# Performance work log

Hardware: AMD Instinct MI355X
Metric: run time of the kernel (lower is better)

Reference implementation:

```python
import jax, jax.numpy as jnp
import numpy as np

N_NODES = 50000
N_EDGES = 800000
N_GRAPHS = 64


def graph_conv(x, edge_index, w_rel, b_rel, w_root):
    # PyG GraphConv with aggr='add':
    #   out = lin_rel(sum_{j in N(i)} x_j) + lin_root(x_i)
    src, dst = edge_index[0], edge_index[1]
    agg = jax.ops.segment_sum(x[src], dst, num_segments=x.shape[0])  # [N, d_in]
    return agg @ w_rel + b_rel + x @ w_root  # [N, d_out]


def scatter_mean(x, batch, num_segments):
    s = jax.ops.segment_sum(x, batch, num_segments=num_segments)
    cnt = jax.ops.segment_sum(jnp.ones((x.shape[0],), x.dtype), batch,
                              num_segments=num_segments)
    return s / jnp.maximum(cnt, 1.0)[:, None]


def setup_inputs() -> dict:
    key = jax.random.key(0)
    ks = jax.random.split(key, 8)
    d_feat, d_hid, d_out = 128, 128, 128
    x = jax.random.normal(ks[0], (N_NODES, d_feat), dtype=jnp.float32)
    edge_index = jax.random.randint(ks[1], (2, N_EDGES), 0, N_NODES, dtype=jnp.int64)
    batch = jnp.sort(jax.random.randint(ks[2], (N_NODES,), 0, N_GRAPHS, dtype=jnp.int64))

    def glorot(k, shape):
        fan_in = shape[0]
        return jax.random.normal(k, shape, dtype=jnp.float32) / np.sqrt(fan_in)

    return {
        "x": x,
        "edge_index": edge_index,
        "batch": batch,
        "w_rel1": glorot(ks[3], (d_feat, d_hid)),
        "b_rel1": jnp.zeros((d_hid,), jnp.float32),
        "w_root1": glorot(ks[4], (d_feat, d_hid)),
        "w_rel2": glorot(ks[5], (d_hid, 2 * d_hid)),
        "b_rel2": jnp.zeros((2 * d_hid,), jnp.float32),
        "w_root2": glorot(ks[6], (d_hid, 2 * d_hid)),
        "w_rel3": glorot(ks[7], (2 * d_hid, d_out)),
        "b_rel3": jnp.zeros((d_out,), jnp.float32),
        "w_root3": glorot(jax.random.fold_in(key, 99), (2 * d_hid, d_out)),
    }


def reference(x, edge_index, batch,
              w_rel1, b_rel1, w_root1,
              w_rel2, b_rel2, w_root2,
              w_rel3, b_rel3, w_root3):
    h = jax.nn.elu(graph_conv(x, edge_index, w_rel1, b_rel1, w_root1))
    h = jax.nn.elu(graph_conv(h, edge_index, w_rel2, b_rel2, w_root2))
    h = jax.nn.elu(graph_conv(h, edge_index, w_rel3, b_rel3, w_root3))
    return scatter_mean(h, batch, N_GRAPHS)  # [num_graphs, n_out]
```

## Files before the change

kernel.cpp:

```cpp
#include <hip/hip_runtime.h>
#include <math.h>

#define NN 50000
#define NNP 50048
#define NE 800000
#define NG 64
#define NBK 196
#define ECH 4082
#define TOTH (NBK * NBK)
#define NBH 151

typedef __attribute__((ext_vector_type(8))) __bf16 bf16x8;
typedef __attribute__((ext_vector_type(8))) short short8;
typedef __attribute__((ext_vector_type(4))) float f32x4;

__device__ inline unsigned short f2bf(float f) {
    unsigned int u = __float_as_uint(f);
    u += 0x7fffu + ((u >> 16) & 1u);
    return (unsigned short)(u >> 16);
}
__device__ inline float bflo(unsigned int v) { return __uint_as_float(v << 16); }
__device__ inline float bfhi(unsigned int v) { return __uint_as_float(v & 0xffff0000u); }
__device__ inline float bfs(unsigned short v) { return __uint_as_float((unsigned int)v << 16); }

#define GLD_LDS16(g, l)                                                          \
    __builtin_amdgcn_global_load_lds(                                            \
        (const __attribute__((address_space(1))) unsigned int*)(g),              \
        (__attribute__((address_space(3))) unsigned int*)(l), 16, 0, 0)

__global__ __launch_bounds__(256) void setup_k(const float* __restrict__ x,
                                               const float* __restrict__ wr1,
                                               const float* __restrict__ wo1,
                                               const float* __restrict__ wr2,
                                               const float* __restrict__ wo2,
                                               const float* __restrict__ wr3,
                                               const float* __restrict__ wo3,
                                               unsigned short* __restrict__ xb,
                                               unsigned short* __restrict__ W1T,
                                               unsigned short* __restrict__ W2T,
                                               unsigned short* __restrict__ W3T) {
    int id = blockIdx.x * 256 + threadIdx.x;
    if (id < NN * 32) {
        float4 v = ((const float4*)x)[id];
        unsigned int p0 = ((unsigned int)f2bf(v.y) << 16) | f2bf(v.x);
        unsigned int p1 = ((unsigned int)f2bf(v.w) << 16) | f2bf(v.z);
        ((uint2*)xb)[id] = make_uint2(p0, p1);
        return;
    }
    int w = id - NN * 32;
    if (w < 32768) {
        int n = w >> 8, k = w & 255;
        W1T[w] = f2bf((k < 128) ? wr1[k * 128 + n] : wo1[(k - 128) * 128 + n]);
    } else if (w < 98304) {
        int j = w - 32768; int n = j >> 8, k = j & 255;
        W2T[j] = f2bf((k < 128) ? wr2[k * 256 + n] : wo2[(k - 128) * 256 + n]);
    } else if (w < 163840) {
        int j = w - 98304; int n = j >> 8, k = j & 255;
        W3T[j] = f2bf((n < 128) ? wr3[k * 128 + n] : wo3[k * 128 + (n - 128)]);
    }
}

__global__ __launch_bounds__(256) void hist_k(const int* __restrict__ dst,
                                              int* __restrict__ H) {
    __shared__ int h[NBK];
    int t = threadIdx.x, k = blockIdx.x;
    if (t < NBK) h[t] = 0;
    __syncthreads();
    int e0 = k * ECH, e1 = min(NE, e0 + ECH);
    for (int e = e0 + t; e < e1; e += 256) atomicAdd(&h[dst[e] >> 8], 1);
    __syncthreads();
    if (t < NBK) H[t * NBK + k] = h[t];
}

__global__ __launch_bounds__(256) void hsum_k(const int* __restrict__ H,
                                              int* __restrict__ hb) {
    int i = blockIdx.x * 256 + threadIdx.x;
    int v = (i < TOTH) ? H[i] : 0;
    for (int off = 32; off; off >>= 1) v += __shfl_xor(v, off, 64);
    __shared__ int ws[4];
    if ((threadIdx.x & 63) == 0) ws[threadIdx.x >> 6] = v;
    __syncthreads();
    if (threadIdx.x == 0) hb[blockIdx.x] = ws[0] + ws[1] + ws[2] + ws[3];
}

__global__ __launch_bounds__(256) void hscan_k(const int* __restrict__ hb,
                                               int* __restrict__ hoff) {
    __shared__ int s[256];
    int t = threadIdx.x;
    int v = (t < NBH) ? hb[t] : 0;
    s[t] = v; __syncthreads();
    for (int off = 1; off < 256; off <<= 1) {
        int u = (t >= off) ? s[t - off] : 0;
        __syncthreads(); s[t] += u; __syncthreads();
    }
    hoff[t] = (t == 0) ? 0 : s[t - 1];
}

__global__ __launch_bounds__(256) void happly_k(const int* __restrict__ H,
                                                const int* __restrict__ hoff,
                                                int* __restrict__ S) {
    int t = threadIdx.x;
    int i = blockIdx.x * 256 + t;
    int v = (i < TOTH) ? H[i] : 0;
    __shared__ int s[256];
    s[t] = v; __syncthreads();
    for (int off = 1; off < 256; off <<= 1) {
        int u = (t >= off) ? s[t - off] : 0;
        __syncthreads(); s[t] += u; __syncthreads();
    }
    if (i < TOTH) S[i] = hoff[blockIdx.x] + s[t] - v;
}

__global__ __launch_bounds__(256) void scatter_k(const int* __restrict__ src,
                                                 const int* __restrict__ dst,
                                                 const int* __restrict__ S,
                                                 int* __restrict__ tmp) {
    __shared__ int cur[NBK];
    int t = threadIdx.x, k = blockIdx.x;
    if (t < NBK) cur[t] = S[t * NBK + k];
    __syncthreads();
    int e0 = k * ECH, e1 = min(NE, e0 + ECH);
    for (int e = e0 + t; e < e1; e += 256) {
        int d = dst[e];
        int p = atomicAdd(&cur[d >> 8], 1);
        tmp[p] = ((d & 255) << 16) | src[e];
    }
}

__global__ __launch_bounds__(256) void csr_k(const int* __restrict__ tmp,
                                             const int* __restrict__ S,
                                             int* __restrict__ rowptr,
                                             int* __restrict__ colsrc) {
    __shared__ int hist[256], off[256], cur[256];
    int t = threadIdx.x, b = blockIdx.x;
    int base = S[b * NBK];
    int next = (b < NBK - 1) ? S[(b + 1) * NBK] : NE;
    int cntb = next - base;
    hist[t] = 0;
    __syncthreads();
    for (int i = t; i < cntb; i += 256) atomicAdd(&hist[tmp[base + i] >> 16], 1);
    __syncthreads();
    int v = hist[t];
    off[t] = v; __syncthreads();
    for (int o = 1; o < 256; o <<= 1) {
        int u = (t >= o) ? off[t - o] : 0;
        __syncthreads(); off[t] += u; __syncthreads();
    }
    int excl = off[t] - v;
    int node = b * 256 + t;
    if (node <= NN) rowptr[node] = base + excl;
    cur[t] = excl;
    __syncthreads();
    for (int i = t; i < cntb; i += 256) {
        int e = tmp[base + i];
        int p = atomicAdd(&cur[e >> 16], 1);
        colsrc[base + p] = e & 0xffff;
    }
}

__global__ __launch_bounds__(256) void aggb_k(const unsigned short* __restrict__ feat,
                                              const int* __restrict__ rowptr,
                                              const int* __restrict__ colsrc,
                                              unsigned short* __restrict__ outp) {
    int node = __builtin_amdgcn_readfirstlane((int)(blockIdx.x * 4 + (threadIdx.x >> 6)));
    int lane = threadIdx.x & 63;
    int beg = rowptr[node], end = rowptr[node + 1];
    float ax = 0.f, ay = 0.f;
    int e = beg;
    for (; e + 4 <= end; e += 4) {
        int s0 = colsrc[e], s1 = colsrc[e + 1], s2 = colsrc[e + 2], s3 = colsrc[e + 3];
        unsigned int v0 = *(const unsigned int*)&feat[(size_t)s0 * 128 + lane * 2];
        unsigned int v1 = *(const unsigned int*)&feat[(size_t)s1 * 128 + lane * 2];
        unsigned int v2 = *(const unsigned int*)&feat[(size_t)s2 * 128 + lane * 2];
        unsigned int v3 = *(const unsigned int*)&feat[(size_t)s3 * 128 + lane * 2];
        ax += bflo(v0); ay += bfhi(v0);
        ax += bflo(v1); ay += bfhi(v1);
        ax += bflo(v2); ay += bfhi(v2);
        ax += bflo(v3); ay += bfhi(v3);
    }
    for (; e < end; ++e) {
        unsigned int v0 = *(const unsigned int*)&feat[(size_t)colsrc[e] * 128 + lane * 2];
        ax += bflo(v0); ay += bfhi(v0);
    }
    unsigned int p = ((unsigned int)f2bf(ay) << 16) | f2bf(ax);
    *(unsigned int*)&outp[(size_t)node * 128 + lane * 2] = p;
}

__global__ __launch_bounds__(256) void aggf_k(const unsigned short* __restrict__ y,
                                              const unsigned short* __restrict__ rr,
                                              const float* __restrict__ b3,
                                              const int* __restrict__ rowptr,
                                              const int* __restrict__ colsrc,
                                              unsigned short* __restrict__ outp) {
    int node = __builtin_amdgcn_readfirstlane((int)(blockIdx.x * 4 + (threadIdx.x >> 6)));
    int lane = threadIdx.x & 63;
    int beg = rowptr[node], end = rowptr[node + 1];
    float ax = 0.f, ay = 0.f;
    int e = beg;
    for (; e + 4 <= end; e += 4) {
        int s0 = colsrc[e], s1 = colsrc[e + 1], s2 = colsrc[e + 2], s3 = colsrc[e + 3];
        unsigned int v0 = *(const unsigned int*)&y[(size_t)s0 * 128 + lane * 2];
        unsigned int v1 = *(const unsigned int*)&y[(size_t)s1 * 128 + lane * 2];
        unsigned int v2 = *(const unsigned int*)&y[(size_t)s2 * 128 + lane * 2];
        unsigned int v3 = *(const unsigned int*)&y[(size_t)s3 * 128 + lane * 2];
        ax += bflo(v0); ay += bfhi(v0);
        ax += bflo(v1); ay += bfhi(v1);
        ax += bflo(v2); ay += bfhi(v2);
        ax += bflo(v3); ay += bfhi(v3);
    }
    for (; e < end; ++e) {
        unsigned int v0 = *(const unsigned int*)&y[(size_t)colsrc[e] * 128 + lane * 2];
        ax += bflo(v0); ay += bfhi(v0);
    }
    unsigned int rv = *(const unsigned int*)&rr[(size_t)node * 128 + lane * 2];
    float2 bb = *(const float2*)&b3[lane * 2];
    float vx = ax + bflo(rv) + bb.x;
    float vy = ay + bfhi(rv) + bb.y;
    vx = vx > 0.f ? vx : (__expf(vx) - 1.f);
    vy = vy > 0.f ? vy : (__expf(vy) - 1.f);
    unsigned int p = ((unsigned int)f2bf(vy) << 16) | f2bf(vx);
    *(unsigned int*)&outp[(size_t)node * 128 + lane * 2] = p;
}

template <int MT, int KA, int N, bool TWO, bool BIAS, bool ELU, bool SPLIT>
__global__ __launch_bounds__(256) void gemm_k(const unsigned short* __restrict__ A1,
                                              const unsigned short* __restrict__ A2,
                                              const unsigned short* __restrict__ WT,
                                              const float* __restrict__ bias,
                                              unsigned short* __restrict__ Cout,
                                              unsigned short* __restrict__ Cout2) {
    constexpr int KTOT = TWO ? 2 * KA : KA;
    constexpr int MI = MT / 32;
    __shared__ __attribute__((aligned(16))) unsigned short As[MT * 32];
    __shared__ __attribute__((aligned(16))) unsigned short Bs[128 * 32];
    const int t = threadIdx.x;
    const int wv = t >> 6, lane = t & 63;
    const int qd = lane >> 4, l16 = lane & 15;
    const int m0 = blockIdx.x * MT, n0 = blockIdx.y * 128;
    const int mh = (wv & 1) * (MT / 2), nh = (wv >> 1) * 64;
    const int srow = lane >> 2;
    const int skk  = (lane & 3) * 8;

    f32x4 acc[MI][4] = {};

    for (int k0 = 0; k0 < KTOT; k0 += 32) {
        const unsigned short* Abase = (TWO && k0 >= KA) ? (A2 + (k0 - KA)) : (A1 + k0);
#pragma unroll
        for (int i = 0; i < MT / 64; ++i) {
            int chunk = wv * (MT / 64) + i;
            const unsigned short* g = Abase + (size_t)(m0 + chunk * 16 + srow) * KA + skk;
            GLD_LDS16(g, &As[chunk * 512]);
        }
        const unsigned short* Wbase = WT + k0;
#pragma unroll
        for (int i = 0; i < 2; ++i) {
            int chunk = wv * 2 + i;
            const unsigned short* g = Wbase + (size_t)(n0 + chunk * 16 + srow) * KTOT + skk;
            GLD_LDS16(g, &Bs[chunk * 512]);
        }
        __syncthreads();
        bf16x8 af[MI], bfr[4];
#pragma unroll
        for (int mi = 0; mi < MI; ++mi)
            af[mi] = *(const bf16x8*)&As[(mh + mi * 16 + l16) * 32 + qd * 8];
#pragma unroll
        for (int ni = 0; ni < 4; ++ni)
            bfr[ni] = *(const bf16x8*)&Bs[(nh + ni * 16 + l16) * 32 + qd * 8];
#pragma unroll
        for (int mi = 0; mi < MI; ++mi)
#pragma unroll
            for (int ni = 0; ni < 4; ++ni)
                acc[mi][ni] = __builtin_amdgcn_mfma_f32_16x16x32_bf16(
                    af[mi], bfr[ni], acc[mi][ni], 0, 0, 0);
        __syncthreads();
    }

#pragma unroll
    for (int mi = 0; mi < MI; ++mi) {
#pragma unroll
        for (int ni = 0; ni < 4; ++ni) {
#pragma unroll
            for (int r = 0; r < 4; ++r) {
                int mm = m0 + mh + mi * 16 + qd * 4 + r;
                if (mm < NN) {
                    int nn = n0 + nh + ni * 16 + l16;
                    float v = acc[mi][ni][r];
                    if (BIAS) v += bias[nn];
                    if (ELU) v = v > 0.f ? v : (__expf(v) - 1.f);
                    unsigned short b = f2bf(v);
                    if (SPLIT) {
                        unsigned short* dst = (nn < 128) ? Cout : Cout2;
                        dst[(size_t)mm * 128 + (nn & 127)] = b;
                    } else {
                        Cout[(size_t)mm * N + nn] = b;
                    }
                }
            }
        }
    }
}

__global__ __launch_bounds__(128) void bounds_k(const int* __restrict__ batch,
                                                int* __restrict__ bounds,
                                                float* __restrict__ outp) {
    int g = threadIdx.x;
    if (g <= NG) {
        int lo = 0, hi = NN;
        while (lo < hi) {
            int mid = (lo + hi) >> 1;
            if (batch[mid] < g) lo = mid + 1; else hi = mid;
        }
        bounds[g] = lo;
    }
    for (int i = threadIdx.x; i < NG * 128; i += 128) outp[i] = 0.f;
}

__global__ __launch_bounds__(128) void sum_k(const unsigned short* __restrict__ vals,
                                             const int* __restrict__ batch,
                                             float* __restrict__ outsum) {
    const int CH = 25;
    int n0 = blockIdx.x * CH;
    int c = threadIdx.x;
    int g = batch[n0];
    float acc = 0.f;
    for (int i = 0; i < CH; ++i) {
        int n = n0 + i;
        int gn = batch[n];
        if (gn != g) {
            unsafeAtomicAdd(&outsum[(size_t)g * 128 + c], acc);
            acc = 0.f; g = gn;
        }
        acc += bfs(vals[(size_t)n * 128 + c]);
    }
    unsafeAtomicAdd(&outsum[(size_t)g * 128 + c], acc);
}

__global__ void divide_k(const int* __restrict__ bounds, float* __restrict__ out) {
    int i = blockIdx.x * 256 + threadIdx.x;
    if (i < NG * 128) {
        int g = i >> 7;
        float c = (float)(bounds[g + 1] - bounds[g]);
        out[i] /= fmaxf(c, 1.f);
    }
}

extern "C" void kernel_launch(void* const* d_in, const int* in_sizes, int n_in,
                              void* d_out, int out_size, void* d_ws, size_t ws_size,
                              hipStream_t stream) {
    const float* x       = (const float*)d_in[0];
    const int*   ei      = (const int*)d_in[1];
    const int*   batch   = (const int*)d_in[2];
    const float* w_rel1  = (const float*)d_in[3];
    const float* b_rel1  = (const float*)d_in[4];
    const float* w_root1 = (const float*)d_in[5];
    const float* w_rel2  = (const float*)d_in[6];
    const float* b_rel2  = (const float*)d_in[7];
    const float* w_root2 = (const float*)d_in[8];
    const float* w_rel3  = (const float*)d_in[9];
    const float* b_rel3  = (const float*)d_in[10];
    const float* w_root3 = (const float*)d_in[11];
    const int* esrc = ei;
    const int* edst = ei + NE;

    unsigned short* Ab = (unsigned short*)d_ws;
    unsigned short* Bb = Ab + (size_t)NNP * 128;
    unsigned short* Cb = Bb + (size_t)NNP * 128;
    unsigned short* xb = Cb + (size_t)NNP * 256;
    unsigned short* W1T = xb + (size_t)NNP * 128;
    unsigned short* W2T = W1T + 128 * 256;
    unsigned short* W3T = W2T + 256 * 256;
    int* rowptr = (int*)(W3T + 256 * 256);
    int* colsrc = rowptr + (NN + 1);
    int* tmp    = colsrc + NE;
    int* H      = tmp + NE;
    int* S      = H + TOTH;
    int* hb     = S + TOTH;
    int* hoff   = hb + 256;
    int* bounds = hoff + 256;
    float* outp = (float*)d_out;

    setup_k<<<(NN * 32 + 163840 + 255) / 256, 256, 0, stream>>>(
        x, w_rel1, w_root1, w_rel2, w_root2, w_rel3, w_root3, xb, W1T, W2T, W3T);
    hist_k<<<NBK, 256, 0, stream>>>(edst, H);
    hsum_k<<<NBH, 256, 0, stream>>>(H, hb);
    hscan_k<<<1, 256, 0, stream>>>(hb, hoff);
    happly_k<<<NBH, 256, 0, stream>>>(H, hoff, S);
    scatter_k<<<NBK, 256, 0, stream>>>(esrc, edst, S, tmp);
    csr_k<<<NBK, 256, 0, stream>>>(tmp, S, rowptr, colsrc);
    bounds_k<<<1, 128, 0, stream>>>(batch, bounds, outp);

    aggb_k<<<NN / 4, 256, 0, stream>>>(xb, rowptr, colsrc, Ab);
    gemm_k<64, 128, 128, true, true, true, false>
        <<<dim3(NNP / 64, 1), 256, 0, stream>>>(Ab, xb, W1T, b_rel1, Bb, nullptr);

    aggb_k<<<NN / 4, 256, 0, stream>>>(Bb, rowptr, colsrc, Ab);
    gemm_k<128, 128, 256, true, true, true, false>
        <<<dim3(NNP / 128, 2), 256, 0, stream>>>(Ab, Bb, W2T, b_rel2, Cb, nullptr);

    gemm_k<128, 256, 256, false, false, false, true>
        <<<dim3(NNP / 128, 2), 256, 0, stream>>>(Cb, nullptr, W3T, nullptr, Ab, Bb);

    aggf_k<<<NN / 4, 256, 0, stream>>>(Ab, Bb, b_rel3, rowptr, colsrc, Cb);
    sum_k<<<NN / 25, 128, 0, stream>>>(Cb, batch, outp);
    divide_k<<<(NG * 128 + 255) / 256, 256, 0, stream>>>(bounds, outp);
}
```

Before: 308.4 us.

## Fuse CSR preprocessing into one cooperative kernel, add 256-wide GEMM, unroll gathers

The chain of setup, histogram, scan, scatter, CSR and bounds kernels is replaced by a single cooperative kernel that uses grid.sync between phases, which removes several launch gaps and raises the histogram chunk count to 1024 blocks. A new gemm256 kernel computes all 256 output columns per 64-row block instead of splitting N across two blocks, so each A tile is loaded once. The gather loops in both aggregation kernels now issue 8 loads per iteration instead of 4, for more memory-level parallelism. The trade-offs are grid-wide barrier costs, a dependence on all 1024 blocks being co-resident, and higher register pressure.

```diff
diff --git a/kernel.cpp b/kernel.cpp
--- a/kernel.cpp
+++ b/kernel.cpp
@@ -1,17 +1,21 @@
 #include <hip/hip_runtime.h>
+#include <hip/hip_cooperative_groups.h>
 #include <math.h>
+
+namespace cg = cooperative_groups;
 
 #define NN 50000
 #define NNP 50048
 #define NE 800000
 #define NG 64
 #define NBK 196
-#define ECH 4082
-#define TOTH (NBK * NBK)
-#define NBH 151
+#define NCHK 1024
+#define ECH2 782
+#define TOT2 (NBK * NCHK)
+#define NSC 784
+#define SWORK (NN * 32 + 163840)
 
 typedef __attribute__((ext_vector_type(8))) __bf16 bf16x8;
-typedef __attribute__((ext_vector_type(8))) short short8;
 typedef __attribute__((ext_vector_type(4))) float f32x4;
 
 __device__ inline unsigned short f2bf(float f) {
@@ -28,133 +32,140 @@
         (const __attribute__((address_space(1))) unsigned int*)(g),              \
         (__attribute__((address_space(3))) unsigned int*)(l), 16, 0, 0)
 
-__global__ __launch_bounds__(256) void setup_k(const float* __restrict__ x,
-                                               const float* __restrict__ wr1,
-                                               const float* __restrict__ wo1,
-                                               const float* __restrict__ wr2,
-                                               const float* __restrict__ wo2,
-                                               const float* __restrict__ wr3,
-                                               const float* __restrict__ wo3,
-                                               unsigned short* __restrict__ xb,
-                                               unsigned short* __restrict__ W1T,
-                                               unsigned short* __restrict__ W2T,
-                                               unsigned short* __restrict__ W3T) {
-    int id = blockIdx.x * 256 + threadIdx.x;
-    if (id < NN * 32) {
-        float4 v = ((const float4*)x)[id];
-        unsigned int p0 = ((unsigned int)f2bf(v.y) << 16) | f2bf(v.x);
-        unsigned int p1 = ((unsigned int)f2bf(v.w) << 16) | f2bf(v.z);
-        ((uint2*)xb)[id] = make_uint2(p0, p1);
-        return;
-    }
-    int w = id - NN * 32;
-    if (w < 32768) {
-        int n = w >> 8, k = w & 255;
-        W1T[w] = f2bf((k < 128) ? wr1[k * 128 + n] : wo1[(k - 128) * 128 + n]);
-    } else if (w < 98304) {
-        int j = w - 32768; int n = j >> 8, k = j & 255;
-        W2T[j] = f2bf((k < 128) ? wr2[k * 256 + n] : wo2[(k - 128) * 256 + n]);
-    } else if (w < 163840) {
-        int j = w - 98304; int n = j >> 8, k = j & 255;
-        W3T[j] = f2bf((n < 128) ? wr3[k * 128 + n] : wo3[k * 128 + (n - 128)]);
-    }
-}
-
-__global__ __launch_bounds__(256) void hist_k(const int* __restrict__ dst,
-                                              int* __restrict__ H) {
-    __shared__ int h[NBK];
-    int t = threadIdx.x, k = blockIdx.x;
-    if (t < NBK) h[t] = 0;
-    __syncthreads();
-    int e0 = k * ECH, e1 = min(NE, e0 + ECH);
-    for (int e = e0 + t; e < e1; e += 256) atomicAdd(&h[dst[e] >> 8], 1);
-    __syncthreads();
-    if (t < NBK) H[t * NBK + k] = h[t];
-}
-
-__global__ __launch_bounds__(256) void hsum_k(const int* __restrict__ H,
-                                              int* __restrict__ hb) {
-    int i = blockIdx.x * 256 + threadIdx.x;
-    int v = (i < TOTH) ? H[i] : 0;
-    for (int off = 32; off; off >>= 1) v += __shfl_xor(v, off, 64);
-    __shared__ int ws[4];
-    if ((threadIdx.x & 63) == 0) ws[threadIdx.x >> 6] = v;
-    __syncthreads();
-    if (threadIdx.x == 0) hb[blockIdx.x] = ws[0] + ws[1] + ws[2] + ws[3];
-}
-
-__global__ __launch_bounds__(256) void hscan_k(const int* __restrict__ hb,
-                                               int* __restrict__ hoff) {
-    __shared__ int s[256];
-    int t = threadIdx.x;
-    int v = (t < NBH) ? hb[t] : 0;
-    s[t] = v; __syncthreads();
-    for (int off = 1; off < 256; off <<= 1) {
-        int u = (t >= off) ? s[t - off] : 0;
-        __syncthreads(); s[t] += u; __syncthreads();
-    }
-    hoff[t] = (t == 0) ? 0 : s[t - 1];
-}
-
-__global__ __launch_bounds__(256) void happly_k(const int* __restrict__ H,
-                                                const int* __restrict__ hoff,
-                                                int* __restrict__ S) {
-    int t = threadIdx.x;
-    int i = blockIdx.x * 256 + t;
-    int v = (i < TOTH) ? H[i] : 0;
-    __shared__ int s[256];
-    s[t] = v; __syncthreads();
-    for (int off = 1; off < 256; off <<= 1) {
-        int u = (t >= off) ? s[t - off] : 0;
-        __syncthreads(); s[t] += u; __syncthreads();
-    }
-    if (i < TOTH) S[i] = hoff[blockIdx.x] + s[t] - v;
-}
-
-__global__ __launch_bounds__(256) void scatter_k(const int* __restrict__ src,
-                                                 const int* __restrict__ dst,
-                                                 const int* __restrict__ S,
-                                                 int* __restrict__ tmp) {
-    __shared__ int cur[NBK];
-    int t = threadIdx.x, k = blockIdx.x;
-    if (t < NBK) cur[t] = S[t * NBK + k];
-    __syncthreads();
-    int e0 = k * ECH, e1 = min(NE, e0 + ECH);
-    for (int e = e0 + t; e < e1; e += 256) {
-        int d = dst[e];
-        int p = atomicAdd(&cur[d >> 8], 1);
-        tmp[p] = ((d & 255) << 16) | src[e];
-    }
-}
-
-__global__ __launch_bounds__(256) void csr_k(const int* __restrict__ tmp,
-                                             const int* __restrict__ S,
-                                             int* __restrict__ rowptr,
-                                             int* __restrict__ colsrc) {
-    __shared__ int hist[256], off[256], cur[256];
-    int t = threadIdx.x, b = blockIdx.x;
-    int base = S[b * NBK];
-    int next = (b < NBK - 1) ? S[(b + 1) * NBK] : NE;
-    int cntb = next - base;
-    hist[t] = 0;
-    __syncthreads();
-    for (int i = t; i < cntb; i += 256) atomicAdd(&hist[tmp[base + i] >> 16], 1);
-    __syncthreads();
-    int v = hist[t];
-    off[t] = v; __syncthreads();
-    for (int o = 1; o < 256; o <<= 1) {
-        int u = (t >= o) ? off[t - o] : 0;
-        __syncthreads(); off[t] += u; __syncthreads();
-    }
-    int excl = off[t] - v;
-    int node = b * 256 + t;
-    if (node <= NN) rowptr[node] = base + excl;
-    cur[t] = excl;
-    __syncthreads();
-    for (int i = t; i < cntb; i += 256) {
-        int e = tmp[base + i];
-        int p = atomicAdd(&cur[e >> 16], 1);
-        colsrc[base + p] = e & 0xffff;
+__global__ __launch_bounds__(256) void prep_k(const float* __restrict__ x,
+                                              const float* __restrict__ wr1,
+                                              const float* __restrict__ wo1,
+                                              const float* __restrict__ wr2,
+                                              const float* __restrict__ wo2,
+                                              const float* __restrict__ wr3,
+                                              const float* __restrict__ wo3,
+                                              const int* __restrict__ esrc,
+                                              const int* __restrict__ edst,
+                                              const int* __restrict__ batch,
+                                              unsigned short* __restrict__ xb,
+                                              unsigned short* __restrict__ W1T,
+                                              unsigned short* __restrict__ W2T,
+                                              unsigned short* __restrict__ W3T,
+                                              int* __restrict__ H,
+                                              int* __restrict__ S,
+                                              int* __restrict__ hb,
+                                              int* __restrict__ tmp,
+                                              int* __restrict__ rowptr,
+                                              int* __restrict__ colsrc,
+                                              int* __restrict__ bounds,
+                                              float* __restrict__ outp) {
+    cg::grid_group grid = cg::this_grid();
+    __shared__ int shm[768];
+    const int t = threadIdx.x, bid = blockIdx.x;
+
+    for (int id = bid * 256 + t; id < SWORK; id += NCHK * 256) {
+        if (id < NN * 32) {
+            float4 v = ((const float4*)x)[id];
+            unsigned int p0 = ((unsigned int)f2bf(v.y) << 16) | f2bf(v.x);
+            unsigned int p1 = ((unsigned int)f2bf(v.w) << 16) | f2bf(v.z);
+            ((uint2*)xb)[id] = make_uint2(p0, p1);
+        } else {
+            int w = id - NN * 32;
+            if (w < 32768) {
+                int n = w >> 8, k = w & 255;
+                W1T[w] = f2bf((k < 128) ? wr1[k * 128 + n] : wo1[(k - 128) * 128 + n]);
+            } else if (w < 98304) {
+                int j = w - 32768; int n = j >> 8, k = j & 255;
+                W2T[j] = f2bf((k < 128) ? wr2[k * 256 + n] : wo2[(k - 128) * 256 + n]);
+            } else {
+                int j = w - 98304; int n = j >> 8, k = j & 255;
+                W3T[j] = f2bf((n < 128) ? wr3[k * 128 + n] : wo3[k * 128 + (n - 128)]);
+            }
+        }
+    }
+    if (bid == 1) { for (int i = t; i < NG * 128; i += 256) outp[i] = 0.f; }
+    if (bid == 2 && t <= NG) {
+        int g = t, lo = 0, hi = NN;
+        while (lo < hi) { int mid = (lo + hi) >> 1; if (batch[mid] < g) lo = mid + 1; else hi = mid; }
+        bounds[g] = lo;
+    }
+    {
+        if (t < NBK) shm[t] = 0;
+        __syncthreads();
+        int e0 = bid * ECH2, e1 = min(NE, e0 + ECH2);
+        for (int e = e0 + t; e < e1; e += 256) atomicAdd(&shm[edst[e] >> 8], 1);
+        __syncthreads();
+        if (t < NBK) H[t * NCHK + bid] = shm[t];
+    }
+    grid.sync();
+
+    for (int c = bid; c < NSC; c += NCHK) {
+        int v = H[c * 256 + t];
+        for (int off = 32; off; off >>= 1) v += __shfl_xor(v, off, 64);
+        if ((t & 63) == 0) shm[t >> 6] = v;
+        __syncthreads();
+        if (t == 0) hb[c] = shm[0] + shm[1] + shm[2] + shm[3];
+        __syncthreads();
+    }
+    grid.sync();
+
+    if (bid == 0) {
+        int v[4], tsum = 0;
+        for (int i = 0; i < 4; ++i) { int c = t * 4 + i; v[i] = (c < NSC) ? hb[c] : 0; tsum += v[i]; }
+        shm[t] = tsum; __syncthreads();
+        for (int off = 1; off < 256; off <<= 1) {
+            int u = (t >= off) ? shm[t - off] : 0;
+            __syncthreads(); shm[t] += u; __syncthreads();
+        }
+        int run = shm[t] - tsum;
+        for (int i = 0; i < 4; ++i) { int c = t * 4 + i; if (c < NSC) { hb[c] = run; run += v[i]; } }
+    }
+    grid.sync();
+
+    for (int c = bid; c < NSC; c += NCHK) {
+        int v = H[c * 256 + t];
+        shm[t] = v; __syncthreads();
+        for (int off = 1; off < 256; off <<= 1) {
+            int u = (t >= off) ? shm[t - off] : 0;
+            __syncthreads(); shm[t] += u; __syncthreads();
+        }
+        S[c * 256 + t] = hb[c] + shm[t] - v;
+        __syncthreads();
+    }
+    grid.sync();
+
+    {
+        if (t < NBK) shm[t] = S[t * NCHK + bid];
+        __syncthreads();
+        int e0 = bid * ECH2, e1 = min(NE, e0 + ECH2);
+        for (int e = e0 + t; e < e1; e += 256) {
+            int d = edst[e];
+            int p = atomicAdd(&shm[d >> 8], 1);
+            tmp[p] = ((d & 255) << 16) | esrc[e];
+        }
+    }
+    grid.sync();
+
+    if (bid < NBK) {
+        int* hist = shm; int* off = shm + 256; int* cur = shm + 512;
+        int base = S[bid * NCHK];
+        int next = (bid < NBK - 1) ? S[(bid + 1) * NCHK] : NE;
+        int cntb = next - base;
+        hist[t] = 0;
+        __syncthreads();
+        for (int i = t; i < cntb; i += 256) atomicAdd(&hist[tmp[base + i] >> 16], 1);
+        __syncthreads();
+        int v = hist[t];
+        off[t] = v; __syncthreads();
+        for (int o = 1; o < 256; o <<= 1) {
+            int u = (t >= o) ? off[t - o] : 0;
+            __syncthreads(); off[t] += u; __syncthreads();
+        }
+        int excl = off[t] - v;
+        int node = bid * 256 + t;
+        if (node <= NN) rowptr[node] = base + excl;
+        cur[t] = excl;
+        __syncthreads();
+        for (int i = t; i < cntb; i += 256) {
+            int e = tmp[base + i];
+            int p = atomicAdd(&cur[e >> 16], 1);
+            colsrc[base + p] = e & 0xffff;
+        }
     }
 }
 
@@ -167,16 +178,13 @@
     int beg = rowptr[node], end = rowptr[node + 1];
     float ax = 0.f, ay = 0.f;
     int e = beg;
-    for (; e + 4 <= end; e += 4) {
-        int s0 = colsrc[e], s1 = colsrc[e + 1], s2 = colsrc[e + 2], s3 = colsrc[e + 3];
-        unsigned int v0 = *(const unsigned int*)&feat[(size_t)s0 * 128 + lane * 2];
-        unsigned int v1 = *(const unsigned int*)&feat[(size_t)s1 * 128 + lane * 2];
-        unsigned int v2 = *(const unsigned int*)&feat[(size_t)s2 * 128 + lane * 2];
-        unsigned int v3 = *(const unsigned int*)&feat[(size_t)s3 * 128 + lane * 2];
-        ax += bflo(v0); ay += bfhi(v0);
-        ax += bflo(v1); ay += bfhi(v1);
-        ax += bflo(v2); ay += bfhi(v2);
-        ax += bflo(v3); ay += bfhi(v3);
+    for (; e + 8 <= end; e += 8) {
+        unsigned int v[8];
+#pragma unroll
+        for (int i = 0; i < 8; ++i)
+            v[i] = *(const unsigned int*)&feat[(size_t)colsrc[e + i] * 128 + lane * 2];
+#pragma unroll
+        for (int i = 0; i < 8; ++i) { ax += bflo(v[i]); ay += bfhi(v[i]); }
     }
     for (; e < end; ++e) {
         unsigned int v0 = *(const unsigned int*)&feat[(size_t)colsrc[e] * 128 + lane * 2];
@@ -197,16 +205,13 @@
     int beg = rowptr[node], end = rowptr[node + 1];
     float ax = 0.f, ay = 0.f;
     int e = beg;
-    for (; e + 4 <= end; e += 4) {
-        int s0 = colsrc[e], s1 = colsrc[e + 1], s2 = colsrc[e + 2], s3 = colsrc[e + 3];
-        unsigned int v0 = *(const unsigned int*)&y[(size_t)s0 * 128 + lane * 2];
-        unsigned int v1 = *(const unsigned int*)&y[(size_t)s1 * 128 + lane * 2];
-        unsigned int v2 = *(const unsigned int*)&y[(size_t)s2 * 128 + lane * 2];
-        unsigned int v3 = *(const unsigned int*)&y[(size_t)s3 * 128 + lane * 2];
-        ax += bflo(v0); ay += bfhi(v0);
-        ax += bflo(v1); ay += bfhi(v1);
-        ax += bflo(v2); ay += bfhi(v2);
-        ax += bflo(v3); ay += bfhi(v3);
+    for (; e + 8 <= end; e += 8) {
+        unsigned int v[8];
+#pragma unroll
+        for (int i = 0; i < 8; ++i)
+            v[i] = *(const unsigned int*)&y[(size_t)colsrc[e + i] * 128 + lane * 2];
+#pragma unroll
+        for (int i = 0; i < 8; ++i) { ax += bflo(v[i]); ay += bfhi(v[i]); }
     }
     for (; e < end; ++e) {
         unsigned int v0 = *(const unsigned int*)&y[(size_t)colsrc[e] * 128 + lane * 2];
@@ -222,13 +227,12 @@
     *(unsigned int*)&outp[(size_t)node * 128 + lane * 2] = p;
 }
 
-template <int MT, int KA, int N, bool TWO, bool BIAS, bool ELU, bool SPLIT>
+template <int MT, int KA, int N, bool TWO, bool BIAS, bool ELU>
 __global__ __launch_bounds__(256) void gemm_k(const unsigned short* __restrict__ A1,
                                               const unsigned short* __restrict__ A2,
                                               const unsigned short* __restrict__ WT,
                                               const float* __restrict__ bias,
-                                              unsigned short* __restrict__ Cout,
-                                              unsigned short* __restrict__ Cout2) {
+                                              unsigned short* __restrict__ Cout) {
     constexpr int KTOT = TWO ? 2 * KA : KA;
     constexpr int MI = MT / 32;
     __shared__ __attribute__((aligned(16))) unsigned short As[MT * 32];
@@ -236,7 +240,7 @@
     const int t = threadIdx.x;
     const int wv = t >> 6, lane = t & 63;
     const int qd = lane >> 4, l16 = lane & 15;
-    const int m0 = blockIdx.x * MT, n0 = blockIdx.y * 128;
+    const int m0 = blockIdx.x * MT, n0 = 0;
     const int mh = (wv & 1) * (MT / 2), nh = (wv >> 1) * 64;
     const int srow = lane >> 2;
     const int skk  = (lane & 3) * 8;
@@ -276,14 +280,80 @@
     }
 
 #pragma unroll
-    for (int mi = 0; mi < MI; ++mi) {
-#pragma unroll
-        for (int ni = 0; ni < 4; ++ni) {
+    for (int mi = 0; mi < MI; ++mi)
+#pragma unroll
+        for (int ni = 0; ni < 4; ++ni)
 #pragma unroll
             for (int r = 0; r < 4; ++r) {
                 int mm = m0 + mh + mi * 16 + qd * 4 + r;
                 if (mm < NN) {
                     int nn = n0 + nh + ni * 16 + l16;
+                    float v = acc[mi][ni][r];
+                    if (BIAS) v += bias[nn];
+                    if (ELU) v = v > 0.f ? v : (__expf(v) - 1.f);
+                    Cout[(size_t)mm * N + nn] = f2bf(v);
+                }
+            }
+}
+
+template <int KA, bool TWO, bool BIAS, bool ELU, bool SPLIT>
+__global__ __launch_bounds__(256) void gemm256_k(const unsigned short* __restrict__ A1,
+                                                 const unsigned short* __restrict__ A2,
+                                                 const unsigned short* __restrict__ WT,
+                                                 const float* __restrict__ bias,
+                                                 unsigned short* __restrict__ Cout,
+                                                 unsigned short* __restrict__ Cout2) {
+    constexpr int KTOT = TWO ? 2 * KA : KA;
+    __shared__ __attribute__((aligned(16))) unsigned short As[64 * 32];
+    __shared__ __attribute__((aligned(16))) unsigned short Bs[256 * 32];
+    const int t = threadIdx.x;
+    const int wv = t >> 6, lane = t & 63;
+    const int qd = lane >> 4, l16 = lane & 15;
+    const int m0 = blockIdx.x * 64;
+    const int srow = lane >> 2;
+    const int skk  = (lane & 3) * 8;
+
+    f32x4 acc[4][4] = {};
+
+    for (int k0 = 0; k0 < KTOT; k0 += 32) {
+        const unsigned short* Abase = (TWO && k0 >= KA) ? (A2 + (k0 - KA)) : (A1 + k0);
+        {
+            const unsigned short* g = Abase + (size_t)(m0 + wv * 16 + srow) * KA + skk;
+            GLD_LDS16(g, &As[wv * 512]);
+        }
+        const unsigned short* Wbase = WT + k0;
+#pragma unroll
+        for (int i = 0; i < 4; ++i) {
+            int chunk = wv * 4 + i;
+            const unsigned short* g = Wbase + (size_t)(chunk * 16 + srow) * KTOT + skk;
+            GLD_LDS16(g, &Bs[chunk * 512]);
+        }
+        __syncthreads();
+        bf16x8 af[4], bfr[4];
+#pragma unroll
+        for (int mi = 0; mi < 4; ++mi)
+            af[mi] = *(const bf16x8*)&As[(mi * 16 + l16) * 32 + qd * 8];
+#pragma unroll
+        for (int ni = 0; ni < 4; ++ni)
+            bfr[ni] = *(const bf16x8*)&Bs[(wv * 64 + ni * 16 + l16) * 32 + qd * 8];
+#pragma unroll
+        for (int mi = 0; mi < 4; ++mi)
+#pragma unroll
+            for (int ni = 0; ni < 4; ++ni)
+                acc[mi][ni] = __builtin_amdgcn_mfma_f32_16x16x32_bf16(
+                    af[mi], bfr[ni], acc[mi][ni], 0, 0, 0);
+        __syncthreads();
+    }
+
+#pragma unroll
+    for (int mi = 0; mi < 4; ++mi)
+#pragma unroll
+        for (int ni = 0; ni < 4; ++ni)
+#pragma unroll
+            for (int r = 0; r < 4; ++r) {
+                int mm = m0 + mi * 16 + qd * 4 + r;
+                if (mm < NN) {
+                    int nn = wv * 64 + ni * 16 + l16;
                     float v = acc[mi][ni][r];
                     if (BIAS) v += bias[nn];
                     if (ELU) v = v > 0.f ? v : (__expf(v) - 1.f);
@@ -292,27 +362,10 @@
                         unsigned short* dst = (nn < 128) ? Cout : Cout2;
                         dst[(size_t)mm * 128 + (nn & 127)] = b;
                     } else {
-                        Cout[(size_t)mm * N + nn] = b;
+                        Cout[(size_t)mm * 256 + nn] = b;
                     }
                 }
             }
-        }
-    }
-}
-
-__global__ __launch_bounds__(128) void bounds_k(const int* __restrict__ batch,
-                                                int* __restrict__ bounds,
-                                                float* __restrict__ outp) {
-    int g = threadIdx.x;
-    if (g <= NG) {
-        int lo = 0, hi = NN;
-        while (lo < hi) {
-            int mid = (lo + hi) >> 1;
-            if (batch[mid] < g) lo = mid + 1; else hi = mid;
-        }
-        bounds[g] = lo;
-    }
-    for (int i = threadIdx.x; i < NG * 128; i += 128) outp[i] = 0.f;
 }
 
 __global__ __launch_bounds__(128) void sum_k(const unsigned short* __restrict__ vals,
@@ -373,32 +426,29 @@
     int* colsrc = rowptr + (NN + 1);
     int* tmp    = colsrc + NE;
     int* H      = tmp + NE;
-    int* S      = H + TOTH;
-    int* hb     = S + TOTH;
-    int* hoff   = hb + 256;
-    int* bounds = hoff + 256;
+    int* S      = H + TOT2;
+    int* hb     = S + TOT2;
+    int* bounds = hb + 1024;
     float* outp = (float*)d_out;
 
-    setup_k<<<(NN * 32 + 163840 + 255) / 256, 256, 0, stream>>>(
-        x, w_rel1, w_root1, w_rel2, w_root2, w_rel3, w_root3, xb, W1T, W2T, W3T);
-    hist_k<<<NBK, 256, 0, stream>>>(edst, H);
-    hsum_k<<<NBH, 256, 0, stream>>>(H, hb);
-    hscan_k<<<1, 256, 0, stream>>>(hb, hoff);
-    happly_k<<<NBH, 256, 0, stream>>>(H, hoff, S);
-    scatter_k<<<NBK, 256, 0, stream>>>(esrc, edst, S, tmp);
-    csr_k<<<NBK, 256, 0, stream>>>(tmp, S, rowptr, colsrc);
-    bounds_k<<<1, 128, 0, stream>>>(batch, bounds, outp);
+    void* args[] = {(void*)&x, (void*)&w_rel1, (void*)&w_root1, (void*)&w_rel2,
+                    (void*)&w_root2, (void*)&w_rel3, (void*)&w_root3,
+                    (void*)&esrc, (void*)&edst, (void*)&batch,
+                    (void*)&xb, (void*)&W1T, (void*)&W2T, (void*)&W3T,
+                    (void*)&H, (void*)&S, (void*)&hb, (void*)&tmp,
+                    (void*)&rowptr, (void*)&colsrc, (void*)&bounds, (void*)&outp};
+    hipLaunchCooperativeKernel((void*)prep_k, dim3(NCHK), dim3(256), args, 0, stream);
 
     aggb_k<<<NN / 4, 256, 0, stream>>>(xb, rowptr, colsrc, Ab);
-    gemm_k<64, 128, 128, true, true, true, false>
-        <<<dim3(NNP / 64, 1), 256, 0, stream>>>(Ab, xb, W1T, b_rel1, Bb, nullptr);
+    gemm_k<64, 128, 128, true, true, true>
+        <<<NNP / 64, 256, 0, stream>>>(Ab, xb, W1T, b_rel1, Bb);
 
     aggb_k<<<NN / 4, 256, 0, stream>>>(Bb, rowptr, colsrc, Ab);
-    gemm_k<128, 128, 256, true, true, true, false>
-        <<<dim3(NNP / 128, 2), 256, 0, stream>>>(Ab, Bb, W2T, b_rel2, Cb, nullptr);
-
-    gemm_k<128, 256, 256, false, false, false, true>
-        <<<dim3(NNP / 128, 2), 256, 0, stream>>>(Cb, nullptr, W3T, nullptr, Ab, Bb);
+    gemm256_k<128, true, true, true, false>
+        <<<NNP / 64, 256, 0, stream>>>(Ab, Bb, W2T, b_rel2, Cb, nullptr);
+
+    gemm256_k<256, false, false, false, true>
+        <<<NNP / 64, 256, 0, stream>>>(Cb, nullptr, W3T, nullptr, Ab, Bb);
 
     aggf_k<<<NN / 4, 256, 0, stream>>>(Ab, Bb, b_rel3, rowptr, colsrc, Cb);
     sum_k<<<NN / 25, 128, 0, stream>>>(Cb, batch, outp);
```

New measurement: 827.0 us. 2.68x slower.
